# Kernel optimization log

Measured on AMD Instinct MI355X. Metric: run time of the kernel, lower is better.

## Reference

```python
import jax, jax.numpy as jnp
import numpy as np

B, C, H, W = 4, 3, 1024, 1024
EPS = 1e-8


def setup_inputs() -> dict:
    key = jax.random.key(0)
    k1, k2 = jax.random.split(key)
    im0 = jax.random.normal(k1, (B, C, H, W), dtype=jnp.float32)
    # grid = identity pixel mesh + small random water-distortion displacement
    yy, xx = jnp.meshgrid(jnp.arange(H, dtype=jnp.float32),
                          jnp.arange(W, dtype=jnp.float32), indexing='ij')
    base = jnp.stack([xx, yy], axis=-1)  # [H,W,2] in (x,y) order
    disp = 2.0 * jax.random.normal(k2, (B, H, W, 2), dtype=jnp.float32)
    grid = base[None] + disp  # [B,H,W,2]
    return {"im0": im0, "grid": grid}


def reference(im0, grid):
    """Forward splatting (griddata): scatter im0 values at coordinates `grid`
    onto the regular HxW grid with bilinear weights, normalized by the
    accumulated weight at each cell."""
    b, c, h, w = im0.shape
    n = h * w
    x = grid[..., 0].reshape(b, n)
    y = grid[..., 1].reshape(b, n)
    x0f = jnp.floor(x)
    y0f = jnp.floor(y)
    dx = x - x0f  # bilinear fractions (differentiable w.r.t. grid)
    dy = y - y0f
    x0 = x0f.astype(jnp.int32)
    y0 = y0f.astype(jnp.int32)

    # 4 corner indices [b,4,n] and bilinear weights
    xs = jnp.stack([x0, x0 + 1, x0, x0 + 1], axis=1)
    ys = jnp.stack([y0, y0, y0 + 1, y0 + 1], axis=1)
    ws = jnp.stack([(1 - dx) * (1 - dy), dx * (1 - dy),
                    (1 - dx) * dy, dx * dy], axis=1)
    valid = (xs >= 0) & (xs < w) & (ys >= 0) & (ys < h)
    ws = ws * valid.astype(ws.dtype)
    idx = (jnp.clip(ys, 0, h - 1) * w + jnp.clip(xs, 0, w - 1)).reshape(b, 4 * n)
    ws = ws.reshape(b, 4 * n)

    vals = im0.reshape(b, c, n)
    contrib = (vals[:, :, None, :] * ws.reshape(b, 1, 4, n)).reshape(b, c, 4 * n)

    def splat(v, wgt, i):
        den = jnp.zeros((n,), wgt.dtype).at[i].add(wgt)
        num = jnp.zeros((c, n), v.dtype).at[:, i].add(v)
        return num / jnp.maximum(den, EPS)[None, :]

    out = jax.vmap(splat)(contrib, ws, idx)  # [b,c,n]
    return out.reshape(b, c, h, w)
```

## Files before the change

### kernel.cpp

```cpp
#include <hip/hip_runtime.h>
#include <hip/hip_fp16.h>

#define B 4
#define C 3
#define H 1024
#define W 1024
#define N (H * W)
#define EPS 1e-8f

#define TW 32
#define TH 32
#define R 8
#define WIN 48
#define NSRC (WIN * WIN)
#define NTASKS (NSRC / 4)
#define BDIM 33
#define NBINS (BDIM * BDIM)
#define NBINW ((NBINS + 1) / 2)
#define K 6
#define NTX (W / TW)
#define NTY (H / TH)
#define NTILES (NTX * NTY * B)

struct OutlierRec { int idx; float dw, d0, d1, d2; };

__global__ __launch_bounds__(256, 3) void splat_gather(
    const float* __restrict__ im0,
    const float* __restrict__ grid,
    float* __restrict__ out,
    float* __restrict__ den,
    int* __restrict__ tileCnt,
    OutlierRec* __restrict__ recs,
    int slots)
{
    __shared__ uint4 rec[NSRC];
    __shared__ unsigned binCntP[NBINW];
    __shared__ unsigned short ent[NBINS * K];

    const int bid = blockIdx.x;
    const int b = bid >> 10;
    const int t = bid & 1023;
    const int tx0 = (t & (NTX - 1)) * TW;
    const int ty0 = (t >> 5) * TH;
    const int tid = threadIdx.x;

    for (int i = tid; i < NBINW; i += 256) binCntP[i] = 0u;
    __syncthreads();

    const int lx0 = tx0 - R;
    const int ly0 = ty0 - R;

    const float* imb   = im0 + (size_t)b * C * N;
    const float* gbase = grid + (size_t)b * N * 2;

    auto push_rec = [&](int xi, int yi, float w, float v0, float v1, float v2) {
        const int tile = (b << 10) | ((yi >> 5) << 5) | (xi >> 5);
        const int slot = atomicAdd(&tileCnt[tile], 1);
        if (slot < slots) {
            OutlierRec r;
            r.idx = b * N + yi * W + xi;
            r.dw = w; r.d0 = v0 * w; r.d1 = v1 * w; r.d2 = v2 * w;
            recs[(size_t)tile * slots + slot] = r;
        }
    };

    for (int task = tid; task < NTASKS; task += 256) {
        const int row = task / (WIN / 4);
        const int col = (task - row * (WIN / 4)) * 4;
        const int sy = ly0 + row;
        const int sxg = lx0 + col;
        if ((unsigned)sy >= H || (unsigned)sxg >= W) continue;

        const int n = sy * W + sxg;
        const float4 g0 = *(const float4*)(gbase + 2 * n);
        const float4 g1 = *(const float4*)(gbase + 2 * n + 4);
        const float4 c0 = *(const float4*)(imb + n);
        const float4 c1 = *(const float4*)(imb + N + n);
        const float4 c2 = *(const float4*)(imb + 2 * N + n);

        const float gxk[4] = {g0.x, g0.z, g1.x, g1.z};
        const float gyk[4] = {g0.y, g0.w, g1.y, g1.w};
        const float v0k[4] = {c0.x, c0.y, c0.z, c0.w};
        const float v1k[4] = {c1.x, c1.y, c1.z, c1.w};
        const float v2k[4] = {c2.x, c2.y, c2.z, c2.w};

#pragma unroll
        for (int k = 0; k < 4; ++k) {
            const int sx = sxg + k;
            const int i = k * NTASKS + task;
            const float gx = gxk[k], gy = gyk[k];
            const float x0f = floorf(gx);
            const float y0f = floorf(gy);
            const float dx = gx - x0f;
            const float dy = gy - y0f;
            const int x0 = (int)x0f;
            const int y0 = (int)y0f;

            {
                uint4 r;
                r.x = __float_as_uint(dx);
                r.y = __float_as_uint(dy);
                __half2 h01 = __floats2half2_rn(v0k[k], v1k[k]);
                r.z = *(unsigned*)&h01;
                __half2 h2 = __floats2half2_rn(v2k[k], 0.f);
                r.w = *(unsigned*)&h2;
                rec[i] = r;
            }

            const int bx = x0 - tx0 + 1;
            const int by = y0 - ty0 + 1;
            if ((unsigned)bx < BDIM && (unsigned)by < BDIM) {
                const int bin = by * BDIM + bx;
                const unsigned sh = (unsigned)(bin & 1) * 16u;
                const unsigned old = atomicAdd(&binCntP[bin >> 1], 1u << sh);
                const unsigned slot = (old >> sh) & 0xffffu;
                if (slot < K) {
                    ent[bin * K + slot] = (unsigned short)i;
                } else {
                    const float wxa[2] = {1.f - dx, dx};
                    const float wya[2] = {1.f - dy, dy};
#pragma unroll
                    for (int cy2 = 0; cy2 < 2; ++cy2)
#pragma unroll
                        for (int cx2 = 0; cx2 < 2; ++cx2) {
                            const int xi = x0 + cx2, yi = y0 + cy2;
                            if ((unsigned)(xi - tx0) < TW &&
                                (unsigned)(yi - ty0) < TH)
                                push_rec(xi, yi, wxa[cx2] * wya[cy2],
                                         v0k[k], v1k[k], v2k[k]);
                        }
                }
            }

            if ((unsigned)(sx - tx0) < TW && (unsigned)(sy - ty0) < TH) {
                const float wxa[2] = {1.f - dx, dx};
                const float wya[2] = {1.f - dy, dy};
#pragma unroll
                for (int cy2 = 0; cy2 < 2; ++cy2)
#pragma unroll
                    for (int cx2 = 0; cx2 < 2; ++cx2) {
                        const int xi = x0 + cx2, yi = y0 + cy2;
                        if ((unsigned)xi < W && (unsigned)yi < H) {
                            const int ox0 = (xi >> 5) << 5;
                            const int oy0 = (yi >> 5) << 5;
                            const bool covered =
                                (sx >= ox0 - R) && (sx < ox0 + TW + R) &&
                                (sy >= oy0 - R) && (sy < oy0 + TH + R);
                            if (!covered)
                                push_rec(xi, yi, wxa[cx2] * wya[cy2],
                                         v0k[k], v1k[k], v2k[k]);
                        }
                    }
            }
        }
    }
    __syncthreads();

    const int cx = tid & 31;
    const int ry = (tid >> 5) * 4;
    float* outb = out + (size_t)b * C * N;
    float* denb = den + (size_t)b * N;

    float d[4]  = {0.f, 0.f, 0.f, 0.f};
    float a0[4] = {0.f, 0.f, 0.f, 0.f};
    float a1[4] = {0.f, 0.f, 0.f, 0.f};
    float a2[4] = {0.f, 0.f, 0.f, 0.f};

#pragma unroll
    for (int s = 0; s < 5; ++s) {
        const int by = ry + s;
#pragma unroll
        for (int jx = 0; jx < 2; ++jx) {
            const int bx = cx + jx;
            const int bin = by * BDIM + bx;
            const unsigned cw = binCntP[bin >> 1];
            const int cnt = min((int)((cw >> ((unsigned)(bin & 1) * 16u)) & 0xffffu), K);
            for (int e = 0; e < cnt; ++e) {
                const int i = ent[bin * K + e];
                const uint4 r = rec[i];
                const float dx = __uint_as_float(r.x);
                const float dy = __uint_as_float(r.y);
                const float2 v01 = __half22float2(*(const __half2*)&r.z);
                const float v2 = __half2float(((const __half2*)&r.w)->x);
                const float wx = jx ? (1.f - dx) : dx;
                if (s > 0) {
                    const float w = wx * (1.f - dy);
                    d[s - 1] += w;
                    a0[s - 1] += v01.x * w;
                    a1[s - 1] += v01.y * w;
                    a2[s - 1] += v2 * w;
                }
                if (s < 4) {
                    const float w = wx * dy;
                    d[s] += w;
                    a0[s] += v01.x * w;
                    a1[s] += v01.y * w;
                    a2[s] += v2 * w;
                }
            }
        }
    }

#pragma unroll
    for (int s = 0; s < 4; ++s) {
        const float inv = 1.f / fmaxf(d[s], EPS);
        const int gi = (ty0 + ry + s) * W + tx0 + cx;
        denb[gi] = d[s];
        outb[gi]         = a0[s] * inv;
        outb[N + gi]     = a1[s] * inv;
        outb[2 * N + gi] = a2[s] * inv;
    }
}

__global__ __launch_bounds__(64) void fix_tiles(
    float* __restrict__ out,
    float* __restrict__ den,
    const int* __restrict__ tileCnt,
    const OutlierRec* __restrict__ recs,
    int slots)
{
    const int bid = blockIdx.x;
    int cnt = tileCnt[bid];
    if (cnt <= 0) return;
    cnt = min(cnt, slots);
    const int tid = threadIdx.x;
    if (tid >= cnt) return;

    OutlierRec rec = recs[(size_t)bid * slots + tid];
    float dw = rec.dw, d0 = rec.d0, d1 = rec.d1, d2 = rec.d2;
    bool first = true;
    for (int r2 = 0; r2 < cnt; ++r2) {
        if (r2 == tid) continue;
        OutlierRec o = recs[(size_t)bid * slots + r2];
        if (o.idx == rec.idx) {
            if (r2 < tid) { first = false; break; }
            dw += o.dw; d0 += o.d0; d1 += o.d1; d2 += o.d2;
        }
    }
    if (!first) return;

    const int b = rec.idx >> 20;
    const int cell = rec.idx & (N - 1);
    float* outb = out + (size_t)b * C * N + cell;
    float* dptr = den + ((size_t)b << 20) + cell;

    float d = *dptr;
    const float m = fmaxf(d, EPS);
    float n0 = outb[0] * m;
    float n1 = outb[N] * m;
    float n2 = outb[2 * N] * m;
    d += dw; n0 += d0; n1 += d1; n2 += d2;
    const float inv = 1.f / fmaxf(d, EPS);
    *dptr = d;
    outb[0]     = n0 * inv;
    outb[N]     = n1 * inv;
    outb[2 * N] = n2 * inv;
}

extern "C" void kernel_launch(void* const* d_in, const int* in_sizes, int n_in,
                              void* d_out, int out_size, void* d_ws, size_t ws_size,
                              hipStream_t stream) {
    const float* im0 = (const float*)d_in[0];
    const float* grid = (const float*)d_in[1];
    float* out = (float*)d_out;

    int* tileCnt = (int*)d_ws;
    float* den = (float*)((char*)d_ws + 16384);
    const size_t rec_off = 16384 + (size_t)B * N * sizeof(float);
    OutlierRec* recs = (OutlierRec*)((char*)d_ws + rec_off);
    int slots = 0;
    if (ws_size > rec_off) {
        size_t avail = (ws_size - rec_off) / sizeof(OutlierRec);
        slots = (int)(avail / NTILES);
        if (slots > 32) slots = 32;
    }

    (void)hipMemsetAsync(tileCnt, 0, NTILES * sizeof(int), stream);

    splat_gather<<<NTILES, 256, 0, stream>>>(im0, grid, out, den,
                                             tileCnt, recs, slots);
    fix_tiles<<<NTILES, 64, 0, stream>>>(out, den, tileCnt, recs, slots);
}
```

Baseline: 175.4 us.

## Compress shared-memory source records and cut bin capacity to raise occupancy

```diff
diff --git a/kernel.cpp b/kernel.cpp
--- a/kernel.cpp
+++ b/kernel.cpp
@@ -17,14 +17,14 @@
 #define BDIM 33
 #define NBINS (BDIM * BDIM)
 #define NBINW ((NBINS + 1) / 2)
-#define K 6
+#define K 5
 #define NTX (W / TW)
 #define NTY (H / TH)
 #define NTILES (NTX * NTY * B)
 
 struct OutlierRec { int idx; float dw, d0, d1, d2; };
 
-__global__ __launch_bounds__(256, 3) void splat_gather(
+__global__ __launch_bounds__(256, 4) void splat_gather(
     const float* __restrict__ im0,
     const float* __restrict__ grid,
     float* __restrict__ out,
@@ -33,9 +33,11 @@
     OutlierRec* __restrict__ recs,
     int slots)
 {
-    __shared__ uint4 rec[NSRC];
+    __shared__ unsigned recW0[NSRC];
+    __shared__ unsigned recW1[NSRC];
+    __shared__ unsigned recW2[NSRC];
     __shared__ unsigned binCntP[NBINW];
-    __shared__ unsigned short ent[NBINS * K];
+    __shared__ unsigned short ent[K * NBINS];
 
     const int bid = blockIdx.x;
     const int b = bid >> 10;
@@ -97,14 +99,15 @@
             const int y0 = (int)y0f;
 
             {
-                uint4 r;
-                r.x = __float_as_uint(dx);
-                r.y = __float_as_uint(dy);
+                unsigned dq = (unsigned)(dx * 65536.0f);
+                unsigned eq = (unsigned)(dy * 65536.0f);
+                if (dq > 65535u) dq = 65535u;
+                if (eq > 65535u) eq = 65535u;
+                recW0[i] = dq | (eq << 16);
                 __half2 h01 = __floats2half2_rn(v0k[k], v1k[k]);
-                r.z = *(unsigned*)&h01;
+                recW1[i] = *(unsigned*)&h01;
                 __half2 h2 = __floats2half2_rn(v2k[k], 0.f);
-                r.w = *(unsigned*)&h2;
-                rec[i] = r;
+                recW2[i] = *(unsigned*)&h2;
             }
 
             const int bx = x0 - tx0 + 1;
@@ -115,7 +118,7 @@
                 const unsigned old = atomicAdd(&binCntP[bin >> 1], 1u << sh);
                 const unsigned slot = (old >> sh) & 0xffffu;
                 if (slot < K) {
-                    ent[bin * K + slot] = (unsigned short)i;
+                    ent[slot * NBINS + bin] = (unsigned short)i;
                 } else {
                     const float wxa[2] = {1.f - dx, dx};
                     const float wya[2] = {1.f - dy, dy};
@@ -176,12 +179,14 @@
             const unsigned cw = binCntP[bin >> 1];
             const int cnt = min((int)((cw >> ((unsigned)(bin & 1) * 16u)) & 0xffffu), K);
             for (int e = 0; e < cnt; ++e) {
-                const int i = ent[bin * K + e];
-                const uint4 r = rec[i];
-                const float dx = __uint_as_float(r.x);
-                const float dy = __uint_as_float(r.y);
-                const float2 v01 = __half22float2(*(const __half2*)&r.z);
-                const float v2 = __half2float(((const __half2*)&r.w)->x);
+                const int i = ent[e * NBINS + bin];
+                const unsigned w0 = recW0[i];
+                const unsigned uv01 = recW1[i];
+                const unsigned uv2 = recW2[i];
+                const float dx = (float)(w0 & 0xffffu) * (1.f / 65536.f);
+                const float dy = (float)(w0 >> 16) * (1.f / 65536.f);
+                const float2 v01 = __half22float2(*(const __half2*)&uv01);
+                const float v2 = __half2float(((const __half2*)&uv2)->x);
                 const float wx = jx ? (1.f - dx) : dx;
                 if (s > 0) {
                     const float w = wx * (1.f - dy);
```

Measured after the change: 171.8 us. 1.02x faster.
